# Kernel optimization log

Measured on AMD Instinct MI355X. Metric: run time of the kernel, lower is better.

## Reference

```python
import jax, jax.numpy as jnp
import numpy as np

N_NODES = 100000
N_EDGES = 3200000
IN_CH = 32
HID = 16


def setup_inputs() -> dict:
    key = jax.random.key(0)
    ks = jax.random.split(key, 8)
    x = jax.random.normal(ks[0], (N_NODES, IN_CH), dtype=jnp.float32)
    edge_index = jax.random.randint(ks[1], (2, N_EDGES), 0, N_NODES, dtype=jnp.int64)
    s1 = 1.0 / np.sqrt(IN_CH)
    s2 = 1.0 / np.sqrt(HID)
    Wl1 = jax.random.normal(ks[2], (HID, IN_CH), dtype=jnp.float32) * s1
    Wr1 = jax.random.normal(ks[3], (HID, IN_CH), dtype=jnp.float32) * s1
    b1 = jnp.zeros((HID,), dtype=jnp.float32)
    Wl2 = jax.random.normal(ks[4], (1, HID), dtype=jnp.float32) * s2
    Wr2 = jax.random.normal(ks[5], (1, HID), dtype=jnp.float32) * s2
    b2 = jnp.zeros((1,), dtype=jnp.float32)
    return {"x": x, "edge_index": edge_index, "Wl1": Wl1, "Wr1": Wr1,
            "b1": b1, "Wl2": Wl2, "Wr2": Wr2, "b2": b2}


def _sage_conv(h, src, dst, deg_inv, Wl, Wr, b):
    # mean aggregation of source features at destination nodes
    msg_sum = jax.ops.segment_sum(h[src], dst, num_segments=N_NODES)  # [N, F]
    agg = msg_sum * deg_inv[:, None]
    # lin_l(agg) + lin_r(h): lin_l carries the bias (PyG SAGEConv convention)
    return agg @ Wl.T + b + h @ Wr.T


def reference(x, edge_index, Wl1, Wr1, b1, Wl2, Wr2, b2):
    src = edge_index[0]
    dst = edge_index[1]
    deg = jax.ops.segment_sum(jnp.ones((N_EDGES,), dtype=x.dtype), dst,
                              num_segments=N_NODES)
    deg_inv = 1.0 / jnp.maximum(deg, 1.0)  # mean; nodes w/o in-edges get 0 agg

    h = _sage_conv(x, src, dst, deg_inv, Wl1, Wr1, b1)
    h = jax.nn.relu(h)
    # F.dropout in eval mode -> identity
    out = _sage_conv(h, src, dst, deg_inv, Wl2, Wr2, b2)
    return out.squeeze(-1)  # [N]
```

## Files before the change

kernel.cpp:

```cpp
#include <hip/hip_runtime.h>

#define N_NODES 100000
#define N_EDGES 3200000
#define NB 1024
#define BKN 98
#define RSZ 3968
#define TILE 6250
#define NTILES 512
#define MAXIT 13
#define MAXB 8


__device__ __forceinline__ float bf2f_lo(unsigned int w) {
  return __uint_as_float(w << 16);
}
__device__ __forceinline__ float bf2f_hi(unsigned int w) {
  return __uint_as_float(w & 0xFFFF0000u);
}
__device__ __forceinline__ unsigned short f2bf(float f) {
  unsigned int b = __float_as_uint(f);
  return (unsigned short)((b + 0x7FFFu + ((b >> 16) & 1u)) >> 16);
}

__global__ __launch_bounds__(256) void k_proj1(
    const float* __restrict__ x, const float* __restrict__ Wl1,
    const float* __restrict__ Wr1, const float* __restrict__ b1,
    unsigned short* __restrict__ p1h, float* __restrict__ q1b,
    int* __restrict__ gcur) {
  __shared__ float sWl[512];
  __shared__ float sWr[512];
  __shared__ float sb[16];
  const int t = threadIdx.x;
  if (t < 64) {
    const int gi = blockIdx.x * 64 + t;
    if (gi < NB * 16) gcur[gi] = 0;
  }
  for (int i = t; i < 512; i += 256) {
    sWl[i] = Wl1[i];
    sWr[i] = Wr1[i];
  }
  if (t < 16) sb[t] = b1[t];
  __syncthreads();

  const int n = blockIdx.x * 256 + t;
  if (n >= N_NODES) return;

  float xr[32];
  const float4* xp = (const float4*)(x + (size_t)n * 32);
#pragma unroll
  for (int j = 0; j < 8; ++j) {
    float4 v = xp[j];
    xr[4 * j + 0] = v.x;
    xr[4 * j + 1] = v.y;
    xr[4 * j + 2] = v.z;
    xr[4 * j + 3] = v.w;
  }
  float pv[16], qv[16];
#pragma unroll
  for (int hh = 0; hh < 16; ++hh) {
    float a = 0.f, b = 0.f;
#pragma unroll
    for (int i = 0; i < 32; ++i) {
      a = fmaf(xr[i], sWl[hh * 32 + i], a);
      b = fmaf(xr[i], sWr[hh * 32 + i], b);
    }
    pv[hh] = a;
    qv[hh] = b + sb[hh];
  }
  unsigned int w[8];
#pragma unroll
  for (int j = 0; j < 8; ++j)
    w[j] = (unsigned int)f2bf(pv[2 * j]) |
           ((unsigned int)f2bf(pv[2 * j + 1]) << 16);
  uint4* pp = (uint4*)(p1h + (size_t)n * 16);
  pp[0] = make_uint4(w[0], w[1], w[2], w[3]);
  pp[1] = make_uint4(w[4], w[5], w[6], w[7]);
  float4* qp = (float4*)(q1b + (size_t)n * 16);
#pragma unroll
  for (int j = 0; j < 4; ++j)
    qp[j] = make_float4(qv[4 * j], qv[4 * j + 1], qv[4 * j + 2], qv[4 * j + 3]);
}

__global__ __launch_bounds__(512) void k_bscatter(const int* __restrict__ ei,
                                                  int* __restrict__ gcur,
                                                  int* __restrict__ recs) {
  __shared__ int hist[1024];
  __shared__ int delta[NB];
  __shared__ int seg[512];
  __shared__ int stage[TILE];
  __shared__ unsigned short bid[TILE + 6];
  const int t = threadIdx.x;
  for (int i = t; i < 1024; i += 512) hist[i] = 0;
  __syncthreads();

  const int tb = blockIdx.x * TILE;
  int rec[MAXIT], aux[MAXIT];
#pragma unroll
  for (int i = 0; i < MAXIT; ++i) {
    const int pos = t + i * 512;
    if (pos < TILE) {
      const int e = tb + pos;
      const int s = ei[e];
      const int d = ei[N_EDGES + e];
      const int k = (int)((unsigned)d / (unsigned)BKN);
      const int rank = atomicAdd(&hist[k], 1);
      rec[i] = ((d - k * BKN) << 17) | s;
      aux[i] = (k << 16) | rank;
    } else {
      aux[i] = -1;
    }
  }
  __syncthreads();

  const int s0 = hist[2 * t], s1 = hist[2 * t + 1];
  const int my = s0 + s1;
  seg[t] = my;
  __syncthreads();
#pragma unroll
  for (int o = 1; o < 512; o <<= 1) {
    const int a = (t >= o) ? seg[t - o] : 0;
    __syncthreads();
    seg[t] += a;
    __syncthreads();
  }
  const int ex = seg[t] - my;
  hist[2 * t] = ex;
  hist[2 * t + 1] = ex + s0;
  {
    const int b = 2 * t;
    if (s0) delta[b] = b * RSZ + atomicAdd(&gcur[b * 16], s0) - ex;
    if (s1)
      delta[b + 1] =
          (b + 1) * RSZ + atomicAdd(&gcur[(b + 1) * 16], s1) - (ex + s0);
  }
  __syncthreads();

#pragma unroll
  for (int i = 0; i < MAXIT; ++i) {
    if (aux[i] >= 0) stage[hist[aux[i] >> 16] + (aux[i] & 0xFFFF)] = rec[i];
  }
  for (int k2 = t; k2 < NB; k2 += 512) {
    const int st = hist[k2];
    const int en = (k2 == NB - 1) ? TILE : hist[k2 + 1];
    for (int p = st; p < en; ++p) bid[p] = (unsigned short)k2;
  }
  __syncthreads();

  for (int pos = t; pos < TILE; pos += 512) {
    const int bb = bid[pos];
    const int idx = delta[bb] + pos;
    if (idx < (bb + 1) * RSZ) recs[idx] = stage[pos];
  }
}

__global__ __launch_bounds__(512, 8) void k_sortagg1(
    const int* __restrict__ gcur, const int* __restrict__ recs,
    const unsigned short* __restrict__ p1h, const float* __restrict__ q1b,
    const float* __restrict__ Wl2, const float* __restrict__ Wr2,
    float* __restrict__ p2, float* __restrict__ r2,
    float* __restrict__ deg_inv) {
  __shared__ int hist[128];
  __shared__ int nstart[128];
  __shared__ int ssort[RSZ];
  __shared__ float sWl[16], sWr[16];
  const int t = threadIdx.x;
  const int kb = blockIdx.x;
  const int b0 = kb * RSZ;
  const int gend = b0 + min(gcur[kb * 16], RSZ);
  if (t < 128) hist[t] = 0;
  if (t < 16) {
    sWl[t] = Wl2[t];
    sWr[t] = Wr2[t];
  }
  __syncthreads();

  int rc[MAXB], ax[MAXB];
#pragma unroll
  for (int i = 0; i < MAXB; ++i) {
    const int r = b0 + t + i * 512;
    if (r < gend) {
      const int rv = recs[r];
      const int local = rv >> 17;
      const int rank = atomicAdd(&hist[local], 1);
      rc[i] = rv & 0x1FFFF;
      ax[i] = (local << 13) | rank;
    } else {
      ax[i] = -1;
    }
  }
  __syncthreads();

  {
    const int v = (t < 128) ? hist[t] : 0;
    if (t < 128) nstart[t] = v;
    __syncthreads();
#pragma unroll
    for (int o = 1; o < 128; o <<= 1) {
      const int a = (t < 128 && t >= o) ? nstart[t - o] : 0;
      __syncthreads();
      if (t < 128) nstart[t] += a;
      __syncthreads();
    }
    if (t < 128) nstart[t] -= v;
  }
  __syncthreads();

#pragma unroll
  for (int i = 0; i < MAXB; ++i) {
    if (ax[i] >= 0) ssort[nstart[ax[i] >> 13] + (ax[i] & 0x1FFF)] = rc[i];
  }
  __syncthreads();

  const int quad = t & 3;
  const int half = quad & 1;
  const int epar = quad >> 1;
  const unsigned short* pb = p1h + half * 8;
  const int local = t >> 2;
  if (local < BKN) {
    const int n = kb * BKN + local;
    if (n < N_NODES) {
      const int st = nstart[local];
      const int k = hist[local];

      float acc[8];
#pragma unroll
      for (int i = 0; i < 8; ++i) acc[i] = 0.f;
      int j = epar;
      for (; j + 6 < k; j += 8) {
        const int s0 = ssort[st + j], s1 = ssort[st + j + 2],
                  s2 = ssort[st + j + 4], s3 = ssort[st + j + 6];
        const uint4 w0 = *(const uint4*)(pb + (size_t)s0 * 16);
        const uint4 w1 = *(const uint4*)(pb + (size_t)s1 * 16);
        const uint4 w2 = *(const uint4*)(pb + (size_t)s2 * 16);
        const uint4 w3 = *(const uint4*)(pb + (size_t)s3 * 16);
        acc[0] +=
            (bf2f_lo(w0.x) + bf2f_lo(w1.x)) + (bf2f_lo(w2.x) + bf2f_lo(w3.x));
        acc[1] +=
            (bf2f_hi(w0.x) + bf2f_hi(w1.x)) + (bf2f_hi(w2.x) + bf2f_hi(w3.x));
        acc[2] +=
            (bf2f_lo(w0.y) + bf2f_lo(w1.y)) + (bf2f_lo(w2.y) + bf2f_lo(w3.y));
        acc[3] +=
            (bf2f_hi(w0.y) + bf2f_hi(w1.y)) + (bf2f_hi(w2.y) + bf2f_hi(w3.y));
        acc[4] +=
            (bf2f_lo(w0.z) + bf2f_lo(w1.z)) + (bf2f_lo(w2.z) + bf2f_lo(w3.z));
        acc[5] +=
            (bf2f_hi(w0.z) + bf2f_hi(w1.z)) + (bf2f_hi(w2.z) + bf2f_hi(w3.z));
        acc[6] +=
            (bf2f_lo(w0.w) + bf2f_lo(w1.w)) + (bf2f_lo(w2.w) + bf2f_lo(w3.w));
        acc[7] +=
            (bf2f_hi(w0.w) + bf2f_hi(w1.w)) + (bf2f_hi(w2.w) + bf2f_hi(w3.w));
      }
      for (; j < k; j += 2) {
        const uint4 w = *(const uint4*)(pb + (size_t)ssort[st + j] * 16);
        acc[0] += bf2f_lo(w.x);
        acc[1] += bf2f_hi(w.x);
        acc[2] += bf2f_lo(w.y);
        acc[3] += bf2f_hi(w.y);
        acc[4] += bf2f_lo(w.z);
        acc[5] += bf2f_hi(w.z);
        acc[6] += bf2f_lo(w.w);
        acc[7] += bf2f_hi(w.w);
      }
#pragma unroll
      for (int i = 0; i < 8; ++i) acc[i] += __shfl_xor(acc[i], 2);

      const float di = 1.f / fmaxf((float)k, 1.f);
      const float4* qp = (const float4*)(q1b + (size_t)n * 16 + half * 8);
      const float4 qa = qp[0], qb = qp[1];
      float h[8];
      h[0] = fmaxf(fmaf(acc[0], di, qa.x), 0.f);
      h[1] = fmaxf(fmaf(acc[1], di, qa.y), 0.f);
      h[2] = fmaxf(fmaf(acc[2], di, qa.z), 0.f);
      h[3] = fmaxf(fmaf(acc[3], di, qa.w), 0.f);
      h[4] = fmaxf(fmaf(acc[4], di, qb.x), 0.f);
      h[5] = fmaxf(fmaf(acc[5], di, qb.y), 0.f);
      h[6] = fmaxf(fmaf(acc[6], di, qb.z), 0.f);
      h[7] = fmaxf(fmaf(acc[7], di, qb.w), 0.f);
      float pa = 0.f, pbv = 0.f;
#pragma unroll
      for (int i = 0; i < 8; ++i) {
        pa = fmaf(h[i], sWl[half * 8 + i], pa);
        pbv = fmaf(h[i], sWr[half * 8 + i], pbv);
      }
      pa += __shfl_xor(pa, 1);
      pbv += __shfl_xor(pbv, 1);
      if (quad == 0) {
        p2[n] = pa;
        r2[n] = pbv;
        deg_inv[n] = di;
      }
    }
  }
}

__global__ __launch_bounds__(512, 8) void k_agg2out(
    const int* __restrict__ gcur, const int* __restrict__ recs,
    const float* __restrict__ p2, const float* __restrict__ r2,
    const float* __restrict__ deg_inv, const float* __restrict__ b2,
    float* __restrict__ out) {
  __shared__ float acc[BKN];
  const int t = threadIdx.x;
  const int kb = blockIdx.x;
  if (t < BKN) acc[t] = 0.f;
  __syncthreads();

  const int b0 = kb * RSZ;
  const int cnt = min(gcur[kb * 16], RSZ);
  int r = t;
  for (; r + 1536 < cnt; r += 2048) {
    const int rv0 = recs[b0 + r];
    const int rv1 = recs[b0 + r + 512];
    const int rv2 = recs[b0 + r + 1024];
    const int rv3 = recs[b0 + r + 1536];
    const float v0 = p2[rv0 & 0x1FFFF];
    const float v1 = p2[rv1 & 0x1FFFF];
    const float v2 = p2[rv2 & 0x1FFFF];
    const float v3 = p2[rv3 & 0x1FFFF];
    atomicAdd(&acc[rv0 >> 17], v0);
    atomicAdd(&acc[rv1 >> 17], v1);
    atomicAdd(&acc[rv2 >> 17], v2);
    atomicAdd(&acc[rv3 >> 17], v3);
  }
  for (; r < cnt; r += 512) {
    const int rv = recs[b0 + r];
    atomicAdd(&acc[rv >> 17], p2[rv & 0x1FFFF]);
  }
  __syncthreads();

  if (t < BKN) {
    const int n = kb * BKN + t;
    if (n < N_NODES) out[n] = fmaf(acc[t], deg_inv[n], r2[n] + b2[0]);
  }
}

extern "C" void kernel_launch(void* const* d_in, const int* in_sizes, int n_in,
                              void* d_out, int out_size, void* d_ws,
                              size_t ws_size, hipStream_t stream) {
  const float* x   = (const float*)d_in[0];
  const int*   ei  = (const int*)d_in[1];
  const float* Wl1 = (const float*)d_in[2];
  const float* Wr1 = (const float*)d_in[3];
  const float* b1  = (const float*)d_in[4];
  const float* Wl2 = (const float*)d_in[5];
  const float* Wr2 = (const float*)d_in[6];
  const float* b2  = (const float*)d_in[7];
  float* out = (float*)d_out;

  const size_t N = N_NODES;
  int* wi = (int*)d_ws;
  int* gcur = wi;
  int* recs = wi + NB * 16;
  unsigned short* p1h = (unsigned short*)(recs + (size_t)NB * RSZ);
  float* q1b     = (float*)(p1h + 16 * N);
  float* p2      = q1b + 16 * N;
  float* r2      = p2 + N;
  float* deg_inv = r2 + N;

  k_proj1<<<(N_NODES + 255) / 256, 256, 0, stream>>>(x, Wl1, Wr1, b1, p1h,
                                                     q1b, gcur);
  k_bscatter<<<NTILES, 512, 0, stream>>>(ei, gcur, recs);
  k_sortagg1<<<NB, 512, 0, stream>>>(gcur, recs, p1h, q1b, Wl2, Wr2, p2, r2,
                                     deg_inv);
  k_agg2out<<<NB, 512, 0, stream>>>(gcur, recs, p2, r2, deg_inv, b2, out);
}
```

Before: 172.0 us.

## Replace atomic bucket cursors with count-scan-scatter pipeline and wavefront scans

The global atomicAdd bucket-cursor scheme is replaced by a deterministic three-pass radix partition. A count pass, fused with the node projection kernel via a block-index split, writes per-tile histograms. A separate scan kernel then computes per-bucket, per-tile offsets and totals, and the scatter kernel uses those offsets instead of global atomics. The shared-memory block scans in the scatter and sort kernels are also rewritten as wavefront shuffle scans to cut barriers. In exchange the edge destination array is read twice and one more kernel launch is added, with extra workspace for the count and offset tables.

Result: slower. 176.4 us (+2.5%).

```diff
diff --git a/kernel.cpp b/kernel.cpp
--- a/kernel.cpp
+++ b/kernel.cpp
@@ -9,6 +9,9 @@
 #define NTILES 512
 #define MAXIT 13
 #define MAXB 8
+#define PROJ_BLOCKS 196
+
+typedef float f32x4 __attribute__((ext_vector_type(4)));
 
 
 __device__ __forceinline__ float bf2f_lo(unsigned int w) {
@@ -22,27 +25,41 @@
   return (unsigned short)((b + 0x7FFFu + ((b >> 16) & 1u)) >> 16);
 }
 
-__global__ __launch_bounds__(256) void k_proj1(
-    const float* __restrict__ x, const float* __restrict__ Wl1,
-    const float* __restrict__ Wr1, const float* __restrict__ b1,
-    unsigned short* __restrict__ p1h, float* __restrict__ q1b,
-    int* __restrict__ gcur) {
-  __shared__ float sWl[512];
-  __shared__ float sWr[512];
-  __shared__ float sb[16];
+__global__ __launch_bounds__(512, 4) void k_countproj(
+    const float* __restrict__ x, const int* __restrict__ ei,
+    const float* __restrict__ Wl1, const float* __restrict__ Wr1,
+    const float* __restrict__ b1, unsigned short* __restrict__ p1h,
+    float* __restrict__ q1b, int* __restrict__ cnt) {
+  __shared__ union {
+    int hist[1024];
+    struct { float Wl[512], Wr[512], b[16]; } w;
+  } u;
   const int t = threadIdx.x;
-  if (t < 64) {
-    const int gi = blockIdx.x * 64 + t;
-    if (gi < NB * 16) gcur[gi] = 0;
-  }
-  for (int i = t; i < 512; i += 256) {
-    sWl[i] = Wl1[i];
-    sWr[i] = Wr1[i];
-  }
-  if (t < 16) sb[t] = b1[t];
-  __syncthreads();
-
-  const int n = blockIdx.x * 256 + t;
+  const int kb = blockIdx.x;
+
+  if (kb < NTILES) {
+    for (int i = t; i < 1024; i += 512) u.hist[i] = 0;
+    __syncthreads();
+    const int tb = kb * TILE;
+#pragma unroll
+    for (int i = 0; i < MAXIT; ++i) {
+      const int pos = t + i * 512;
+      if (pos < TILE) {
+        const int d = ei[N_EDGES + tb + pos];
+        atomicAdd(&u.hist[(int)((unsigned)d / (unsigned)BKN)], 1);
+      }
+    }
+    __syncthreads();
+    ((int2*)(cnt + kb * NB))[t] = make_int2(u.hist[2 * t], u.hist[2 * t + 1]);
+    return;
+  }
+
+  u.w.Wl[t] = Wl1[t];
+  u.w.Wr[t] = Wr1[t];
+  if (t < 16) u.w.b[t] = b1[t];
+  __syncthreads();
+
+  const int n = (kb - NTILES) * 512 + t;
   if (n >= N_NODES) return;
 
   float xr[32];
@@ -61,11 +78,11 @@
     float a = 0.f, b = 0.f;
 #pragma unroll
     for (int i = 0; i < 32; ++i) {
-      a = fmaf(xr[i], sWl[hh * 32 + i], a);
-      b = fmaf(xr[i], sWr[hh * 32 + i], b);
+      a = fmaf(xr[i], u.w.Wl[hh * 32 + i], a);
+      b = fmaf(xr[i], u.w.Wr[hh * 32 + i], b);
     }
     pv[hh] = a;
-    qv[hh] = b + sb[hh];
+    qv[hh] = b + u.w.b[hh];
   }
   unsigned int w[8];
 #pragma unroll
@@ -81,19 +98,43 @@
     qp[j] = make_float4(qv[4 * j], qv[4 * j + 1], qv[4 * j + 2], qv[4 * j + 3]);
 }
 
-__global__ __launch_bounds__(512) void k_bscatter(const int* __restrict__ ei,
-                                                  int* __restrict__ gcur,
-                                                  int* __restrict__ recs) {
+__global__ __launch_bounds__(512) void k_scan(const int* __restrict__ cnt,
+                                              int* __restrict__ offs,
+                                              int* __restrict__ tot) {
+  const int t = threadIdx.x;
+  const int lane = t & 63;
+  const int b = blockIdx.x * 8 + (t >> 6);
+  int carry = 0;
+#pragma unroll
+  for (int c = 0; c < 8; ++c) {
+    const int tile = c * 64 + lane;
+    const int v = cnt[tile * NB + b];
+    int incl = v;
+#pragma unroll
+    for (int o = 1; o < 64; o <<= 1) {
+      const int uu = __shfl_up(incl, o);
+      if (lane >= o) incl += uu;
+    }
+    offs[b * NTILES + tile] = carry + incl - v;
+    carry += __shfl(incl, 63);
+  }
+  if (lane == 0) tot[b] = carry;
+}
+
+__global__ __launch_bounds__(512, 4) void k_scatter(const int* __restrict__ ei,
+                                                    const int* __restrict__ offs,
+                                                    int* __restrict__ recs) {
   __shared__ int hist[1024];
   __shared__ int delta[NB];
-  __shared__ int seg[512];
+  __shared__ int wsum[8];
   __shared__ int stage[TILE];
   __shared__ unsigned short bid[TILE + 6];
   const int t = threadIdx.x;
+  const int kb = blockIdx.x;
   for (int i = t; i < 1024; i += 512) hist[i] = 0;
   __syncthreads();
 
-  const int tb = blockIdx.x * TILE;
+  const int tb = kb * TILE;
   int rec[MAXIT], aux[MAXIT];
 #pragma unroll
   for (int i = 0; i < MAXIT; ++i) {
@@ -113,25 +154,32 @@
   __syncthreads();
 
   const int s0 = hist[2 * t], s1 = hist[2 * t + 1];
-  const int my = s0 + s1;
-  seg[t] = my;
-  __syncthreads();
-#pragma unroll
-  for (int o = 1; o < 512; o <<= 1) {
-    const int a = (t >= o) ? seg[t - o] : 0;
-    __syncthreads();
-    seg[t] += a;
-    __syncthreads();
-  }
-  const int ex = seg[t] - my;
+  const int sp = s0 + s1;
+  int incl = sp;
+#pragma unroll
+  for (int o = 1; o < 64; o <<= 1) {
+    const int uu = __shfl_up(incl, o);
+    if ((t & 63) >= o) incl += uu;
+  }
+  if ((t & 63) == 63) wsum[t >> 6] = incl;
+  __syncthreads();
+  if (t == 0) {
+    int run = 0;
+#pragma unroll
+    for (int i = 0; i < 8; ++i) {
+      const int v = wsum[i];
+      wsum[i] = run;
+      run += v;
+    }
+  }
+  __syncthreads();
+  const int ex = wsum[t >> 6] + incl - sp;
   hist[2 * t] = ex;
   hist[2 * t + 1] = ex + s0;
   {
     const int b = 2 * t;
-    if (s0) delta[b] = b * RSZ + atomicAdd(&gcur[b * 16], s0) - ex;
-    if (s1)
-      delta[b + 1] =
-          (b + 1) * RSZ + atomicAdd(&gcur[(b + 1) * 16], s1) - (ex + s0);
+    delta[b] = b * RSZ + offs[b * NTILES + kb] - ex;
+    delta[b + 1] = (b + 1) * RSZ + offs[(b + 1) * NTILES + kb] - (ex + s0);
   }
   __syncthreads();
 
@@ -154,7 +202,7 @@
 }
 
 __global__ __launch_bounds__(512, 8) void k_sortagg1(
-    const int* __restrict__ gcur, const int* __restrict__ recs,
+    const int* __restrict__ tot, const int* __restrict__ recs,
     const unsigned short* __restrict__ p1h, const float* __restrict__ q1b,
     const float* __restrict__ Wl2, const float* __restrict__ Wr2,
     float* __restrict__ p2, float* __restrict__ r2,
@@ -166,7 +214,7 @@
   const int t = threadIdx.x;
   const int kb = blockIdx.x;
   const int b0 = kb * RSZ;
-  const int gend = b0 + min(gcur[kb * 16], RSZ);
+  const int cend = min(tot[kb], RSZ);
   if (t < 128) hist[t] = 0;
   if (t < 16) {
     sWl[t] = Wl2[t];
@@ -177,9 +225,9 @@
   int rc[MAXB], ax[MAXB];
 #pragma unroll
   for (int i = 0; i < MAXB; ++i) {
-    const int r = b0 + t + i * 512;
-    if (r < gend) {
-      const int rv = recs[r];
+    const int r = t + i * 512;
+    if (r < cend) {
+      const int rv = recs[b0 + r];
       const int local = rv >> 17;
       const int rank = atomicAdd(&hist[local], 1);
       rc[i] = rv & 0x1FFFF;
@@ -190,18 +238,21 @@
   }
   __syncthreads();
 
-  {
-    const int v = (t < 128) ? hist[t] : 0;
-    if (t < 128) nstart[t] = v;
-    __syncthreads();
-#pragma unroll
-    for (int o = 1; o < 128; o <<= 1) {
-      const int a = (t < 128 && t >= o) ? nstart[t - o] : 0;
-      __syncthreads();
-      if (t < 128) nstart[t] += a;
-      __syncthreads();
-    }
-    if (t < 128) nstart[t] -= v;
+  if (t < 64) {
+    const int a = hist[t], b = hist[t + 64];
+    int ia = a, ib = b;
+#pragma unroll
+    for (int o = 1; o < 64; o <<= 1) {
+      const int ua = __shfl_up(ia, o);
+      const int ub = __shfl_up(ib, o);
+      if (t >= o) {
+        ia += ua;
+        ib += ub;
+      }
+    }
+    const int tt = __shfl(ia, 63);
+    nstart[t] = ia - a;
+    nstart[t + 64] = tt + ib - b;
   }
   __syncthreads();
 
@@ -294,7 +345,7 @@
 }
 
 __global__ __launch_bounds__(512, 8) void k_agg2out(
-    const int* __restrict__ gcur, const int* __restrict__ recs,
+    const int* __restrict__ tot, const int* __restrict__ recs,
     const float* __restrict__ p2, const float* __restrict__ r2,
     const float* __restrict__ deg_inv, const float* __restrict__ b2,
     float* __restrict__ out) {
@@ -305,7 +356,7 @@
   __syncthreads();
 
   const int b0 = kb * RSZ;
-  const int cnt = min(gcur[kb * 16], RSZ);
+  const int cnt = min(tot[kb], RSZ);
   int r = t;
   for (; r + 1536 < cnt; r += 2048) {
     const int rv0 = recs[b0 + r];
@@ -348,18 +399,21 @@
 
   const size_t N = N_NODES;
   int* wi = (int*)d_ws;
-  int* gcur = wi;
-  int* recs = wi + NB * 16;
+  int* cnt  = wi;
+  int* offs = cnt + NTILES * NB;
+  int* tot  = offs + NB * NTILES;
+  int* recs = tot + NB;
   unsigned short* p1h = (unsigned short*)(recs + (size_t)NB * RSZ);
   float* q1b     = (float*)(p1h + 16 * N);
   float* p2      = q1b + 16 * N;
   float* r2      = p2 + N;
   float* deg_inv = r2 + N;
 
-  k_proj1<<<(N_NODES + 255) / 256, 256, 0, stream>>>(x, Wl1, Wr1, b1, p1h,
-                                                     q1b, gcur);
-  k_bscatter<<<NTILES, 512, 0, stream>>>(ei, gcur, recs);
-  k_sortagg1<<<NB, 512, 0, stream>>>(gcur, recs, p1h, q1b, Wl2, Wr2, p2, r2,
+  k_countproj<<<NTILES + PROJ_BLOCKS, 512, 0, stream>>>(x, ei, Wl1, Wr1, b1,
+                                                        p1h, q1b, cnt);
+  k_scan<<<NB / 8, 512, 0, stream>>>(cnt, offs, tot);
+  k_scatter<<<NTILES, 512, 0, stream>>>(ei, offs, recs);
+  k_sortagg1<<<NB, 512, 0, stream>>>(tot, recs, p1h, q1b, Wl2, Wr2, p2, r2,
                                      deg_inv);
-  k_agg2out<<<NB, 512, 0, stream>>>(gcur, recs, p2, r2, deg_inv, b2, out);
-}
+  k_agg2out<<<NB, 512, 0, stream>>>(tot, recs, p2, r2, deg_inv, b2, out);
+}
```

## Pad bucket segments to 16-record chunks with hole records for vectorized int4 access

Applied to the files above, without the earlier changes.

The bucket scatter now uses 1024-thread blocks over larger tiles. It counts destinations in a first pass, then reserves bucket space in multiples of 16 records and writes aligned int4 chunks padded with hole records, replacing the staged per-element scatter. Downstream sort and aggregation kernels read records as int4 and use wavefront shuffle scans instead of barrier-heavy shared scans. Hole records land in local slot 127, which is why the accumulator is widened to 128. The cost is reading the edge destinations twice, extra padding traffic, a larger per-bucket region, and a risk of overflow truncation if padded counts exceed RSZ.

Measured after the change: 175.8 us. 1.02x slower.

```diff
diff --git a/kernel.cpp b/kernel.cpp
--- a/kernel.cpp
+++ b/kernel.cpp
@@ -4,11 +4,11 @@
 #define N_EDGES 3200000
 #define NB 1024
 #define BKN 98
-#define RSZ 3968
-#define TILE 6250
-#define NTILES 512
-#define MAXIT 13
-#define MAXB 8
+#define RSZ 5120
+#define TILE 12500
+#define NTILES 256
+#define MAXB4 3
+#define HOLE_REC (127 << 17)
 
 
 __device__ __forceinline__ float bf2f_lo(unsigned int w) {
@@ -81,75 +81,87 @@
     qp[j] = make_float4(qv[4 * j], qv[4 * j + 1], qv[4 * j + 2], qv[4 * j + 3]);
 }
 
-__global__ __launch_bounds__(512) void k_bscatter(const int* __restrict__ ei,
-                                                  int* __restrict__ gcur,
-                                                  int* __restrict__ recs) {
+__global__ __launch_bounds__(1024, 1) void k_bscatter(
+    const int* __restrict__ ei, int* __restrict__ gcur,
+    int* __restrict__ recs) {
   __shared__ int hist[1024];
-  __shared__ int delta[NB];
-  __shared__ int seg[512];
+  __shared__ int bstart[1024];
+  __shared__ int gbase[1024];
+  __shared__ int wsum[16];
   __shared__ int stage[TILE];
-  __shared__ unsigned short bid[TILE + 6];
   const int t = threadIdx.x;
-  for (int i = t; i < 1024; i += 512) hist[i] = 0;
-  __syncthreads();
-
-  const int tb = blockIdx.x * TILE;
-  int rec[MAXIT], aux[MAXIT];
-#pragma unroll
-  for (int i = 0; i < MAXIT; ++i) {
-    const int pos = t + i * 512;
+  const int kb = blockIdx.x;
+  hist[t] = 0;
+  __syncthreads();
+
+  const int tb = kb * TILE;
+#pragma unroll
+  for (int i = 0; i < 13; ++i) {
+    const int pos = t + i * 1024;
+    if (pos < TILE) {
+      const int d = ei[N_EDGES + tb + pos];
+      atomicAdd(&hist[(int)((unsigned)d / (unsigned)BKN)], 1);
+    }
+  }
+  __syncthreads();
+
+  const int sv = hist[t];
+  int incl = sv;
+#pragma unroll
+  for (int o = 1; o < 64; o <<= 1) {
+    const int uu = __shfl_up(incl, o);
+    if ((t & 63) >= o) incl += uu;
+  }
+  if ((t & 63) == 63) wsum[t >> 6] = incl;
+  __syncthreads();
+  if (t == 0) {
+    int run = 0;
+#pragma unroll
+    for (int i = 0; i < 16; ++i) {
+      const int v = wsum[i];
+      wsum[i] = run;
+      run += v;
+    }
+  }
+  __syncthreads();
+  bstart[t] = wsum[t >> 6] + incl - sv;
+  {
+    const int pc = (sv + 15) & ~15;
+    gbase[t] = pc ? atomicAdd(&gcur[t * 16], pc) : 0;
+  }
+  hist[t] = 0;
+  __syncthreads();
+
+#pragma unroll
+  for (int i = 0; i < 13; ++i) {
+    const int pos = t + i * 1024;
     if (pos < TILE) {
       const int e = tb + pos;
       const int s = ei[e];
       const int d = ei[N_EDGES + e];
       const int k = (int)((unsigned)d / (unsigned)BKN);
-      const int rank = atomicAdd(&hist[k], 1);
-      rec[i] = ((d - k * BKN) << 17) | s;
-      aux[i] = (k << 16) | rank;
-    } else {
-      aux[i] = -1;
-    }
-  }
-  __syncthreads();
-
-  const int s0 = hist[2 * t], s1 = hist[2 * t + 1];
-  const int my = s0 + s1;
-  seg[t] = my;
-  __syncthreads();
-#pragma unroll
-  for (int o = 1; o < 512; o <<= 1) {
-    const int a = (t >= o) ? seg[t - o] : 0;
-    __syncthreads();
-    seg[t] += a;
-    __syncthreads();
-  }
-  const int ex = seg[t] - my;
-  hist[2 * t] = ex;
-  hist[2 * t + 1] = ex + s0;
+      const int r = atomicAdd(&hist[k], 1);
+      stage[bstart[k] + r] = ((d - k * BKN) << 17) | s;
+    }
+  }
+  __syncthreads();
+
   {
-    const int b = 2 * t;
-    if (s0) delta[b] = b * RSZ + atomicAdd(&gcur[b * 16], s0) - ex;
-    if (s1)
-      delta[b + 1] =
-          (b + 1) * RSZ + atomicAdd(&gcur[(b + 1) * 16], s1) - (ex + s0);
-  }
-  __syncthreads();
-
-#pragma unroll
-  for (int i = 0; i < MAXIT; ++i) {
-    if (aux[i] >= 0) stage[hist[aux[i] >> 16] + (aux[i] & 0xFFFF)] = rec[i];
-  }
-  for (int k2 = t; k2 < NB; k2 += 512) {
-    const int st = hist[k2];
-    const int en = (k2 == NB - 1) ? TILE : hist[k2 + 1];
-    for (int p = st; p < en; ++p) bid[p] = (unsigned short)k2;
-  }
-  __syncthreads();
-
-  for (int pos = t; pos < TILE; pos += 512) {
-    const int bb = bid[pos];
-    const int idx = delta[bb] + pos;
-    if (idx < (bb + 1) * RSZ) recs[idx] = stage[pos];
+    const int c = hist[t];
+    const int st = bstart[t];
+    const int off = gbase[t];
+    const int pc = (c + 15) & ~15;
+    int* gb = recs + (size_t)t * RSZ + off;
+    for (int i = 0; i < pc; i += 4) {
+      if (off + i + 4 <= RSZ) {
+        int4 v;
+        v.x = (i < c) ? stage[st + i] : HOLE_REC;
+        v.y = (i + 1 < c) ? stage[st + i + 1] : HOLE_REC;
+        v.z = (i + 2 < c) ? stage[st + i + 2] : HOLE_REC;
+        v.w = (i + 3 < c) ? stage[st + i + 3] : HOLE_REC;
+        *(int4*)(gb + i) = v;
+      }
+    }
   }
 }
 
@@ -165,8 +177,8 @@
   __shared__ float sWl[16], sWr[16];
   const int t = threadIdx.x;
   const int kb = blockIdx.x;
-  const int b0 = kb * RSZ;
-  const int gend = b0 + min(gcur[kb * 16], RSZ);
+  const int cend = min(gcur[kb * 16], RSZ);
+  const int n4 = cend >> 2;
   if (t < 128) hist[t] = 0;
   if (t < 16) {
     sWl[t] = Wl2[t];
@@ -174,39 +186,48 @@
   }
   __syncthreads();
 
-  int rc[MAXB], ax[MAXB];
-#pragma unroll
-  for (int i = 0; i < MAXB; ++i) {
-    const int r = b0 + t + i * 512;
-    if (r < gend) {
-      const int rv = recs[r];
-      const int local = rv >> 17;
-      const int rank = atomicAdd(&hist[local], 1);
-      rc[i] = rv & 0x1FFFF;
-      ax[i] = (local << 13) | rank;
+  const int4* r4 = (const int4*)(recs + (size_t)kb * RSZ);
+  int rc[12], ax[12];
+#pragma unroll
+  for (int i = 0; i < MAXB4; ++i) {
+    const int idx = t + i * 512;
+    if (idx < n4) {
+      const int4 v = r4[idx];
+      const int l0 = v.x >> 17, l1 = v.y >> 17, l2 = v.z >> 17, l3 = v.w >> 17;
+      rc[4 * i + 0] = v.x & 0x1FFFF;
+      ax[4 * i + 0] = (l0 << 13) | atomicAdd(&hist[l0], 1);
+      rc[4 * i + 1] = v.y & 0x1FFFF;
+      ax[4 * i + 1] = (l1 << 13) | atomicAdd(&hist[l1], 1);
+      rc[4 * i + 2] = v.z & 0x1FFFF;
+      ax[4 * i + 2] = (l2 << 13) | atomicAdd(&hist[l2], 1);
+      rc[4 * i + 3] = v.w & 0x1FFFF;
+      ax[4 * i + 3] = (l3 << 13) | atomicAdd(&hist[l3], 1);
     } else {
-      ax[i] = -1;
-    }
-  }
-  __syncthreads();
-
-  {
-    const int v = (t < 128) ? hist[t] : 0;
-    if (t < 128) nstart[t] = v;
-    __syncthreads();
-#pragma unroll
-    for (int o = 1; o < 128; o <<= 1) {
-      const int a = (t < 128 && t >= o) ? nstart[t - o] : 0;
-      __syncthreads();
-      if (t < 128) nstart[t] += a;
-      __syncthreads();
-    }
-    if (t < 128) nstart[t] -= v;
-  }
-  __syncthreads();
-
-#pragma unroll
-  for (int i = 0; i < MAXB; ++i) {
+      ax[4 * i + 0] = ax[4 * i + 1] = ax[4 * i + 2] = ax[4 * i + 3] = -1;
+    }
+  }
+  __syncthreads();
+
+  if (t < 64) {
+    const int a = hist[t], b = hist[t + 64];
+    int ia = a, ib = b;
+#pragma unroll
+    for (int o = 1; o < 64; o <<= 1) {
+      const int ua = __shfl_up(ia, o);
+      const int ub = __shfl_up(ib, o);
+      if (t >= o) {
+        ia += ua;
+        ib += ub;
+      }
+    }
+    const int tt = __shfl(ia, 63);
+    nstart[t] = ia - a;
+    nstart[t + 64] = tt + ib - b;
+  }
+  __syncthreads();
+
+#pragma unroll
+  for (int i = 0; i < 12; ++i) {
     if (ax[i] >= 0) ssort[nstart[ax[i] >> 13] + (ax[i] & 0x1FFF)] = rc[i];
   }
   __syncthreads();
@@ -298,32 +319,29 @@
     const float* __restrict__ p2, const float* __restrict__ r2,
     const float* __restrict__ deg_inv, const float* __restrict__ b2,
     float* __restrict__ out) {
-  __shared__ float acc[BKN];
+  __shared__ float acc[128];
   const int t = threadIdx.x;
   const int kb = blockIdx.x;
-  if (t < BKN) acc[t] = 0.f;
-  __syncthreads();
-
-  const int b0 = kb * RSZ;
-  const int cnt = min(gcur[kb * 16], RSZ);
-  int r = t;
-  for (; r + 1536 < cnt; r += 2048) {
-    const int rv0 = recs[b0 + r];
-    const int rv1 = recs[b0 + r + 512];
-    const int rv2 = recs[b0 + r + 1024];
-    const int rv3 = recs[b0 + r + 1536];
-    const float v0 = p2[rv0 & 0x1FFFF];
-    const float v1 = p2[rv1 & 0x1FFFF];
-    const float v2 = p2[rv2 & 0x1FFFF];
-    const float v3 = p2[rv3 & 0x1FFFF];
-    atomicAdd(&acc[rv0 >> 17], v0);
-    atomicAdd(&acc[rv1 >> 17], v1);
-    atomicAdd(&acc[rv2 >> 17], v2);
-    atomicAdd(&acc[rv3 >> 17], v3);
-  }
-  for (; r < cnt; r += 512) {
-    const int rv = recs[b0 + r];
-    atomicAdd(&acc[rv >> 17], p2[rv & 0x1FFFF]);
+  if (t < 128) acc[t] = 0.f;
+  __syncthreads();
+
+  const int cend = min(gcur[kb * 16], RSZ);
+  const int n4 = cend >> 2;
+  const int4* r4 = (const int4*)(recs + (size_t)kb * RSZ);
+#pragma unroll
+  for (int i = 0; i < MAXB4; ++i) {
+    const int idx = t + i * 512;
+    if (idx < n4) {
+      const int4 v = r4[idx];
+      const float p0 = p2[v.x & 0x1FFFF];
+      const float p1 = p2[v.y & 0x1FFFF];
+      const float pz = p2[v.z & 0x1FFFF];
+      const float pw = p2[v.w & 0x1FFFF];
+      atomicAdd(&acc[v.x >> 17], p0);
+      atomicAdd(&acc[v.y >> 17], p1);
+      atomicAdd(&acc[v.z >> 17], pz);
+      atomicAdd(&acc[v.w >> 17], pw);
+    }
   }
   __syncthreads();
 
@@ -358,7 +376,7 @@
 
   k_proj1<<<(N_NODES + 255) / 256, 256, 0, stream>>>(x, Wl1, Wr1, b1, p1h,
                                                      q1b, gcur);
-  k_bscatter<<<NTILES, 512, 0, stream>>>(ei, gcur, recs);
+  k_bscatter<<<NTILES, 1024, 0, stream>>>(ei, gcur, recs);
   k_sortagg1<<<NB, 512, 0, stream>>>(gcur, recs, p1h, q1b, Wl2, Wr2, p2, r2,
                                      deg_inv);
   k_agg2out<<<NB, 512, 0, stream>>>(gcur, recs, p2, r2, deg_inv, b2, out);
```

## Replace per-bucket counting sort with shared-memory float atomic accumulation in layer-1 aggregation

Applied to the files above, without the earlier changes.

The layer-1 aggregation kernel no longer counting-sorts each bucket's edge records by destination before gathering. Each thread now gathers the full 16-wide bf16 source row for each record and adds it into a shared-memory accumulator (16 x 100 floats) with LDS float atomics, counting degree with an integer atomic. This removes the histogram/prefix-scan/scatter phases and their barriers, and every edge gathers a full row at once. In exchange it issues 16 shared atomics per edge, which may contend on the same destination, and summation order becomes nondeterministic.

New measurement: 415.4 us. +141.5%, slower.

```diff
diff --git a/kernel.cpp b/kernel.cpp
--- a/kernel.cpp
+++ b/kernel.cpp
@@ -8,7 +8,7 @@
 #define TILE 6250
 #define NTILES 512
 #define MAXIT 13
-#define MAXB 8
+#define ACCS 100
 
 
 __device__ __forceinline__ float bf2f_lo(unsigned int w) {
@@ -153,20 +153,18 @@
   }
 }
 
-__global__ __launch_bounds__(512, 8) void k_sortagg1(
+__global__ __launch_bounds__(512, 8) void k_agg1(
     const int* __restrict__ gcur, const int* __restrict__ recs,
     const unsigned short* __restrict__ p1h, const float* __restrict__ q1b,
     const float* __restrict__ Wl2, const float* __restrict__ Wr2,
     float* __restrict__ p2, float* __restrict__ r2,
     float* __restrict__ deg_inv) {
+  __shared__ float sacc[16 * ACCS];
   __shared__ int hist[128];
-  __shared__ int nstart[128];
-  __shared__ int ssort[RSZ];
   __shared__ float sWl[16], sWr[16];
   const int t = threadIdx.x;
   const int kb = blockIdx.x;
-  const int b0 = kb * RSZ;
-  const int gend = b0 + min(gcur[kb * 16], RSZ);
+  for (int i = t; i < 16 * ACCS; i += 512) sacc[i] = 0.f;
   if (t < 128) hist[t] = 0;
   if (t < 16) {
     sWl[t] = Wl2[t];
@@ -174,108 +172,100 @@
   }
   __syncthreads();
 
-  int rc[MAXB], ax[MAXB];
-#pragma unroll
-  for (int i = 0; i < MAXB; ++i) {
-    const int r = b0 + t + i * 512;
-    if (r < gend) {
-      const int rv = recs[r];
-      const int local = rv >> 17;
-      const int rank = atomicAdd(&hist[local], 1);
-      rc[i] = rv & 0x1FFFF;
-      ax[i] = (local << 13) | rank;
-    } else {
-      ax[i] = -1;
-    }
-  }
-  __syncthreads();
-
-  {
-    const int v = (t < 128) ? hist[t] : 0;
-    if (t < 128) nstart[t] = v;
-    __syncthreads();
-#pragma unroll
-    for (int o = 1; o < 128; o <<= 1) {
-      const int a = (t < 128 && t >= o) ? nstart[t - o] : 0;
-      __syncthreads();
-      if (t < 128) nstart[t] += a;
-      __syncthreads();
-    }
-    if (t < 128) nstart[t] -= v;
-  }
-  __syncthreads();
-
-#pragma unroll
-  for (int i = 0; i < MAXB; ++i) {
-    if (ax[i] >= 0) ssort[nstart[ax[i] >> 13] + (ax[i] & 0x1FFF)] = rc[i];
-  }
-  __syncthreads();
-
-  const int quad = t & 3;
-  const int half = quad & 1;
-  const int epar = quad >> 1;
-  const unsigned short* pb = p1h + half * 8;
-  const int local = t >> 2;
+  const int b0 = kb * RSZ;
+  const int cend = min(gcur[kb * 16], RSZ);
+
+  int r = t;
+  for (; r + 512 < cend; r += 1024) {
+    const int rv0 = recs[b0 + r];
+    const int rv1 = recs[b0 + r + 512];
+    const int l0 = rv0 >> 17, l1 = rv1 >> 17;
+    const uint4* pa = (const uint4*)(p1h + (size_t)(rv0 & 0x1FFFF) * 16);
+    const uint4* pc = (const uint4*)(p1h + (size_t)(rv1 & 0x1FFFF) * 16);
+    const uint4 a0 = pa[0], a1 = pa[1];
+    const uint4 c0 = pc[0], c1 = pc[1];
+    atomicAdd(&hist[l0], 1);
+    atomicAdd(&hist[l1], 1);
+    float* s0 = sacc + l0;
+    float* s1 = sacc + l1;
+    atomicAdd(s0 + 0 * ACCS, bf2f_lo(a0.x));
+    atomicAdd(s0 + 1 * ACCS, bf2f_hi(a0.x));
+    atomicAdd(s0 + 2 * ACCS, bf2f_lo(a0.y));
+    atomicAdd(s0 + 3 * ACCS, bf2f_hi(a0.y));
+    atomicAdd(s0 + 4 * ACCS, bf2f_lo(a0.z));
+    atomicAdd(s0 + 5 * ACCS, bf2f_hi(a0.z));
+    atomicAdd(s0 + 6 * ACCS, bf2f_lo(a0.w));
+    atomicAdd(s0 + 7 * ACCS, bf2f_hi(a0.w));
+    atomicAdd(s0 + 8 * ACCS, bf2f_lo(a1.x));
+    atomicAdd(s0 + 9 * ACCS, bf2f_hi(a1.x));
+    atomicAdd(s0 + 10 * ACCS, bf2f_lo(a1.y));
+    atomicAdd(s0 + 11 * ACCS, bf2f_hi(a1.y));
+    atomicAdd(s0 + 12 * ACCS, bf2f_lo(a1.z));
+    atomicAdd(s0 + 13 * ACCS, bf2f_hi(a1.z));
+    atomicAdd(s0 + 14 * ACCS, bf2f_lo(a1.w));
+    atomicAdd(s0 + 15 * ACCS, bf2f_hi(a1.w));
+    atomicAdd(s1 + 0 * ACCS, bf2f_lo(c0.x));
+    atomicAdd(s1 + 1 * ACCS, bf2f_hi(c0.x));
+    atomicAdd(s1 + 2 * ACCS, bf2f_lo(c0.y));
+    atomicAdd(s1 + 3 * ACCS, bf2f_hi(c0.y));
+    atomicAdd(s1 + 4 * ACCS, bf2f_lo(c0.z));
+    atomicAdd(s1 + 5 * ACCS, bf2f_hi(c0.z));
+    atomicAdd(s1 + 6 * ACCS, bf2f_lo(c0.w));
+    atomicAdd(s1 + 7 * ACCS, bf2f_hi(c0.w));
+    atomicAdd(s1 + 8 * ACCS, bf2f_lo(c1.x));
+    atomicAdd(s1 + 9 * ACCS, bf2f_hi(c1.x));
+    atomicAdd(s1 + 10 * ACCS, bf2f_lo(c1.y));
+    atomicAdd(s1 + 11 * ACCS, bf2f_hi(c1.y));
+    atomicAdd(s1 + 12 * ACCS, bf2f_lo(c1.z));
+    atomicAdd(s1 + 13 * ACCS, bf2f_hi(c1.z));
+    atomicAdd(s1 + 14 * ACCS, bf2f_lo(c1.w));
+    atomicAdd(s1 + 15 * ACCS, bf2f_hi(c1.w));
+  }
+  if (r < cend) {
+    const int rv0 = recs[b0 + r];
+    const int l0 = rv0 >> 17;
+    const uint4* pa = (const uint4*)(p1h + (size_t)(rv0 & 0x1FFFF) * 16);
+    const uint4 a0 = pa[0], a1 = pa[1];
+    atomicAdd(&hist[l0], 1);
+    float* s0 = sacc + l0;
+    atomicAdd(s0 + 0 * ACCS, bf2f_lo(a0.x));
+    atomicAdd(s0 + 1 * ACCS, bf2f_hi(a0.x));
+    atomicAdd(s0 + 2 * ACCS, bf2f_lo(a0.y));
+    atomicAdd(s0 + 3 * ACCS, bf2f_hi(a0.y));
+    atomicAdd(s0 + 4 * ACCS, bf2f_lo(a0.z));
+    atomicAdd(s0 + 5 * ACCS, bf2f_hi(a0.z));
+    atomicAdd(s0 + 6 * ACCS, bf2f_lo(a0.w));
+    atomicAdd(s0 + 7 * ACCS, bf2f_hi(a0.w));
+    atomicAdd(s0 + 8 * ACCS, bf2f_lo(a1.x));
+    atomicAdd(s0 + 9 * ACCS, bf2f_hi(a1.x));
+    atomicAdd(s0 + 10 * ACCS, bf2f_lo(a1.y));
+    atomicAdd(s0 + 11 * ACCS, bf2f_hi(a1.y));
+    atomicAdd(s0 + 12 * ACCS, bf2f_lo(a1.z));
+    atomicAdd(s0 + 13 * ACCS, bf2f_hi(a1.z));
+    atomicAdd(s0 + 14 * ACCS, bf2f_lo(a1.w));
+    atomicAdd(s0 + 15 * ACCS, bf2f_hi(a1.w));
+  }
+  __syncthreads();
+
+  const int half = t & 1;
+  const int local = t >> 1;
   if (local < BKN) {
     const int n = kb * BKN + local;
     if (n < N_NODES) {
-      const int st = nstart[local];
       const int k = hist[local];
-
-      float acc[8];
-#pragma unroll
-      for (int i = 0; i < 8; ++i) acc[i] = 0.f;
-      int j = epar;
-      for (; j + 6 < k; j += 8) {
-        const int s0 = ssort[st + j], s1 = ssort[st + j + 2],
-                  s2 = ssort[st + j + 4], s3 = ssort[st + j + 6];
-        const uint4 w0 = *(const uint4*)(pb + (size_t)s0 * 16);
-        const uint4 w1 = *(const uint4*)(pb + (size_t)s1 * 16);
-        const uint4 w2 = *(const uint4*)(pb + (size_t)s2 * 16);
-        const uint4 w3 = *(const uint4*)(pb + (size_t)s3 * 16);
-        acc[0] +=
-            (bf2f_lo(w0.x) + bf2f_lo(w1.x)) + (bf2f_lo(w2.x) + bf2f_lo(w3.x));
-        acc[1] +=
-            (bf2f_hi(w0.x) + bf2f_hi(w1.x)) + (bf2f_hi(w2.x) + bf2f_hi(w3.x));
-        acc[2] +=
-            (bf2f_lo(w0.y) + bf2f_lo(w1.y)) + (bf2f_lo(w2.y) + bf2f_lo(w3.y));
-        acc[3] +=
-            (bf2f_hi(w0.y) + bf2f_hi(w1.y)) + (bf2f_hi(w2.y) + bf2f_hi(w3.y));
-        acc[4] +=
-            (bf2f_lo(w0.z) + bf2f_lo(w1.z)) + (bf2f_lo(w2.z) + bf2f_lo(w3.z));
-        acc[5] +=
-            (bf2f_hi(w0.z) + bf2f_hi(w1.z)) + (bf2f_hi(w2.z) + bf2f_hi(w3.z));
-        acc[6] +=
-            (bf2f_lo(w0.w) + bf2f_lo(w1.w)) + (bf2f_lo(w2.w) + bf2f_lo(w3.w));
-        acc[7] +=
-            (bf2f_hi(w0.w) + bf2f_hi(w1.w)) + (bf2f_hi(w2.w) + bf2f_hi(w3.w));
-      }
-      for (; j < k; j += 2) {
-        const uint4 w = *(const uint4*)(pb + (size_t)ssort[st + j] * 16);
-        acc[0] += bf2f_lo(w.x);
-        acc[1] += bf2f_hi(w.x);
-        acc[2] += bf2f_lo(w.y);
-        acc[3] += bf2f_hi(w.y);
-        acc[4] += bf2f_lo(w.z);
-        acc[5] += bf2f_hi(w.z);
-        acc[6] += bf2f_lo(w.w);
-        acc[7] += bf2f_hi(w.w);
-      }
-#pragma unroll
-      for (int i = 0; i < 8; ++i) acc[i] += __shfl_xor(acc[i], 2);
-
       const float di = 1.f / fmaxf((float)k, 1.f);
       const float4* qp = (const float4*)(q1b + (size_t)n * 16 + half * 8);
       const float4 qa = qp[0], qb = qp[1];
+      const float* sa = sacc + local + half * 8 * ACCS;
       float h[8];
-      h[0] = fmaxf(fmaf(acc[0], di, qa.x), 0.f);
-      h[1] = fmaxf(fmaf(acc[1], di, qa.y), 0.f);
-      h[2] = fmaxf(fmaf(acc[2], di, qa.z), 0.f);
-      h[3] = fmaxf(fmaf(acc[3], di, qa.w), 0.f);
-      h[4] = fmaxf(fmaf(acc[4], di, qb.x), 0.f);
-      h[5] = fmaxf(fmaf(acc[5], di, qb.y), 0.f);
-      h[6] = fmaxf(fmaf(acc[6], di, qb.z), 0.f);
-      h[7] = fmaxf(fmaf(acc[7], di, qb.w), 0.f);
+      h[0] = fmaxf(fmaf(sa[0 * ACCS], di, qa.x), 0.f);
+      h[1] = fmaxf(fmaf(sa[1 * ACCS], di, qa.y), 0.f);
+      h[2] = fmaxf(fmaf(sa[2 * ACCS], di, qa.z), 0.f);
+      h[3] = fmaxf(fmaf(sa[3 * ACCS], di, qa.w), 0.f);
+      h[4] = fmaxf(fmaf(sa[4 * ACCS], di, qb.x), 0.f);
+      h[5] = fmaxf(fmaf(sa[5 * ACCS], di, qb.y), 0.f);
+      h[6] = fmaxf(fmaf(sa[6 * ACCS], di, qb.z), 0.f);
+      h[7] = fmaxf(fmaf(sa[7 * ACCS], di, qb.w), 0.f);
       float pa = 0.f, pbv = 0.f;
 #pragma unroll
       for (int i = 0; i < 8; ++i) {
@@ -284,7 +274,7 @@
       }
       pa += __shfl_xor(pa, 1);
       pbv += __shfl_xor(pbv, 1);
-      if (quad == 0) {
+      if (half == 0) {
         p2[n] = pa;
         r2[n] = pbv;
         deg_inv[n] = di;
@@ -359,7 +349,7 @@
   k_proj1<<<(N_NODES + 255) / 256, 256, 0, stream>>>(x, Wl1, Wr1, b1, p1h,
                                                      q1b, gcur);
   k_bscatter<<<NTILES, 512, 0, stream>>>(ei, gcur, recs);
-  k_sortagg1<<<NB, 512, 0, stream>>>(gcur, recs, p1h, q1b, Wl2, Wr2, p2, r2,
-                                     deg_inv);
+  k_agg1<<<NB, 512, 0, stream>>>(gcur, recs, p1h, q1b, Wl2, Wr2, p2, r2,
+                                 deg_inv);
   k_agg2out<<<NB, 512, 0, stream>>>(gcur, recs, p2, r2, deg_inv, b2, out);
 }
```
